# Optimization experiments

Measured on AMD Instinct MI355X. Metric: run time of the kernel, lower is better.

The kernel has to match this reference:

```python
import jax, jax.numpy as jnp
import numpy as np
import math

D = 1024
B, S = 4, 4096


def setup_inputs() -> dict:
    key = jax.random.key(0)
    ks = jax.random.split(key, 8)
    x = jax.random.normal(ks[0], (B, S, D), dtype=jnp.float32)
    W_omega = jax.random.normal(ks[1], (D, D), dtype=jnp.float32) * (1.0 / math.sqrt(D))
    b_omega = jnp.zeros((D,), dtype=jnp.float32)
    log_scale = jnp.full((D,), math.log(0.1), dtype=jnp.float32)
    ln_gamma = jnp.ones((4 * D,), dtype=jnp.float32)
    ln_beta = jnp.zeros((4 * D,), dtype=jnp.float32)
    W1 = jax.random.normal(ks[2], (4 * D, 2 * D), dtype=jnp.float32) * (1.0 / math.sqrt(4 * D))
    b1 = jnp.zeros((2 * D,), dtype=jnp.float32)
    W2 = jax.random.normal(ks[3], (2 * D, D), dtype=jnp.float32) * (1.0 / math.sqrt(2 * D))
    b2 = jnp.zeros((D,), dtype=jnp.float32)
    return {"x": x, "W_omega": W_omega, "b_omega": b_omega, "log_scale": log_scale,
            "ln_gamma": ln_gamma, "ln_beta": ln_beta, "W1": W1, "b1": b1, "W2": W2, "b2": b2}


def _layernorm(x, gamma, beta, eps=1e-5):
    mu = jnp.mean(x, axis=-1, keepdims=True)
    var = jnp.var(x, axis=-1, keepdims=True)
    return (x - mu) * jax.lax.rsqrt(var + eps) * gamma + beta


def reference(x, W_omega, b_omega, log_scale, ln_gamma, ln_beta, W1, b1, W2, b2):
    # x: (B, S, D)
    seq_len = x.shape[1]
    omega = jnp.einsum('bsd,de->bse', x, W_omega) + b_omega
    position = jnp.arange(1, seq_len + 1, dtype=x.dtype)[None, :, None]  # (1,S,1)
    pos_scale = 1.0 / jnp.sqrt(position)
    scale = jnp.exp(log_scale)
    omega_scaled = omega * scale * pos_scale
    phi = jnp.cumsum(omega_scaled, axis=1)
    cos_phi = jnp.cos(phi)
    sin_phi = jnp.sin(phi)
    content_real = x * cos_phi
    content_imag = x * sin_phi
    mem_real = jnp.cumsum(content_real, axis=1) / position
    mem_imag = jnp.cumsum(content_imag, axis=1) / position
    retrieved_real = mem_real * cos_phi + mem_imag * sin_phi
    retrieved_imag = mem_imag * cos_phi - mem_real * sin_phi
    context = jnp.concatenate([content_real, content_imag, retrieved_real, retrieved_imag], axis=-1)
    h = _layernorm(context, ln_gamma, ln_beta)
    h = jnp.einsum('bsf,fg->bsg', h, W1) + b1
    h = jax.nn.gelu(h, approximate=False)  # torch GELU default is exact erf
    # dropout is identity in eval mode
    phase_contribution = jnp.einsum('bsg,gd->bsd', h, W2) + b2
    return x + phase_contribution
```

## Files before the change

kernel.cpp:

```cpp
#include <hip/hip_runtime.h>
#include <hip/hip_bf16.h>
#include <math.h>

typedef __hip_bfloat16 bf16;
typedef __attribute__((ext_vector_type(8))) short bf16x8;
typedef __attribute__((ext_vector_type(4))) float f32x4;

static constexpr int DD = 1024;
static constexpr int BB = 4;
static constexpr int SS = 4096;
static constexpr int FD = 4096;
static constexpr int GDIM = 2048;
static constexpr long SD = (long)SS * DD;
static constexpr long SD4 = 4 * SD;

__device__ __forceinline__ void gl2lds16(const bf16* g, bf16* l) {
    __builtin_amdgcn_global_load_lds(
        (const __attribute__((address_space(1))) void*)g,
        (__attribute__((address_space(3))) void*)l, 16, 0, 0);
}

template <int EPI>
__global__ __launch_bounds__(512, 2) void gemm256(
    const bf16* __restrict__ A, const bf16* __restrict__ BT, void* __restrict__ Cp,
    const float* __restrict__ bias, const float* __restrict__ Xadd,
    int M, int N, int K, long strA, long strBT, long strC)
{
    extern __shared__ bf16 lds[];
    const int tid = threadIdx.x;
    const int l = tid & 63, wv = tid >> 6;
    const int wr = wv >> 2, wc = wv & 3;

    int lin = blockIdx.y * gridDim.x + blockIdx.x;
    {
        const int nwg = gridDim.x * gridDim.y;
        const int qq = nwg >> 3, rr = nwg & 7;
        const int xcd = lin & 7, idx = lin >> 3;
        lin = (xcd < rr ? xcd * (qq + 1) : rr * (qq + 1) + (xcd - rr) * qq) + idx;
    }
    const long m0 = (long)(lin / gridDim.x) * 256;
    const long n0 = (long)(lin % gridDim.x) * 256;

    A += (long)blockIdx.z * strA;
    BT += (long)blockIdx.z * strBT;

    const int schunk = (tid & 3) ^ ((tid >> 3) & 3);
    const bf16* pa = A + (m0 + (tid >> 2)) * (long)K + schunk * 8;
    const bf16* pb = BT + (n0 + (tid >> 2)) * (long)K + schunk * 8;
    const long rowK = 128L * (long)K;
    const int stgOff = wv * 512;

    const int fm = l & 15, q = l >> 4;
    const int lof = fm * 32 + ((q ^ ((fm >> 1) & 3)) * 8);

    f32x4 acc[8][4];
#pragma unroll
    for (int i = 0; i < 8; ++i)
#pragma unroll
        for (int j = 0; j < 4; ++j) acc[i][j] = (f32x4){0.f, 0.f, 0.f, 0.f};

    const int NT = K >> 6;

    {
        bf16* dA0 = lds + stgOff;
        bf16* dA1 = lds + 8192 + stgOff;
        bf16* dB0 = lds + 32768 + stgOff;
        bf16* dB1 = lds + 40960 + stgOff;
        gl2lds16(pa, dA0);       gl2lds16(pa + rowK, dA0 + 4096);
        gl2lds16(pb, dB0);       gl2lds16(pb + rowK, dB0 + 4096);
        gl2lds16(pa + 32, dA1);  gl2lds16(pa + 32 + rowK, dA1 + 4096);
        gl2lds16(pb + 32, dB1);  gl2lds16(pb + 32 + rowK, dB1 + 4096);
        asm volatile("s_waitcnt vmcnt(4)" ::: "memory");
        __builtin_amdgcn_s_barrier();
    }

    for (int t = 0; t < NT; ++t) {
        const int buf = t & 1;
        const bool more = (t + 1) < NT;
        const long ko = (long)(t + 1) * 64;
        const bf16* As0 = lds + buf * 16384;
        const bf16* As1 = As0 + 8192;
        const bf16* Bs0 = lds + 32768 + buf * 16384;
        const bf16* Bs1 = Bs0 + 8192;
        bf16* nA0 = lds + (buf ^ 1) * 16384 + stgOff;
        bf16* nA1 = nA0 + 8192;
        bf16* nB0 = lds + 32768 + (buf ^ 1) * 16384 + stgOff;
        bf16* nB1 = nB0 + 8192;

        {
            const bf16* bb = Bs0 + (wc * 64) * 32 + lof;
            const bf16* ab = As0 + (wr * 128) * 32 + lof;
            bf16x8 bq[4], a0[4], a1[4];
#pragma unroll
            for (int j = 0; j < 4; ++j) bq[j] = *(const bf16x8*)(bb + j * 512);
#pragma unroll
            for (int i = 0; i < 4; ++i) a0[i] = *(const bf16x8*)(ab + i * 512);
#pragma unroll
            for (int i = 0; i < 4; ++i) a1[i] = *(const bf16x8*)(ab + 64 * 32 + i * 512);
            if (more) {
                gl2lds16(pa + ko, nA0); gl2lds16(pa + ko + rowK, nA0 + 4096);
                gl2lds16(pb + ko, nB0); gl2lds16(pb + ko + rowK, nB0 + 4096);
            }
            __builtin_amdgcn_s_setprio(1);
#pragma unroll
            for (int i = 0; i < 4; ++i)
#pragma unroll
                for (int j = 0; j < 4; ++j)
                    acc[i][j] = __builtin_amdgcn_mfma_f32_16x16x32_bf16(a0[i], bq[j], acc[i][j], 0, 0, 0);
            __builtin_amdgcn_s_setprio(0);
            if (more) { gl2lds16(pa + ko + 32, nA1); gl2lds16(pa + ko + 32 + rowK, nA1 + 4096); }
            __builtin_amdgcn_s_setprio(1);
#pragma unroll
            for (int i = 0; i < 4; ++i)
#pragma unroll
                for (int j = 0; j < 4; ++j)
                    acc[4 + i][j] = __builtin_amdgcn_mfma_f32_16x16x32_bf16(a1[i], bq[j], acc[4 + i][j], 0, 0, 0);
            __builtin_amdgcn_s_setprio(0);
        }
        if (more) asm volatile("s_waitcnt vmcnt(6)" ::: "memory");
        else      asm volatile("s_waitcnt vmcnt(0)" ::: "memory");
        __builtin_amdgcn_s_barrier();

        {
            const bf16* bb = Bs1 + (wc * 64) * 32 + lof;
            const bf16* ab = As1 + (wr * 128) * 32 + lof;
            bf16x8 bq[4], a0[4], a1[4];
#pragma unroll
            for (int j = 0; j < 4; ++j) bq[j] = *(const bf16x8*)(bb + j * 512);
#pragma unroll
            for (int i = 0; i < 4; ++i) a0[i] = *(const bf16x8*)(ab + i * 512);
#pragma unroll
            for (int i = 0; i < 4; ++i) a1[i] = *(const bf16x8*)(ab + 64 * 32 + i * 512);
            if (more) { gl2lds16(pb + ko + 32, nB1); gl2lds16(pb + ko + 32 + rowK, nB1 + 4096); }
            __builtin_amdgcn_s_setprio(1);
#pragma unroll
            for (int i = 0; i < 4; ++i)
#pragma unroll
                for (int j = 0; j < 4; ++j)
                    acc[i][j] = __builtin_amdgcn_mfma_f32_16x16x32_bf16(a0[i], bq[j], acc[i][j], 0, 0, 0);
            __builtin_amdgcn_s_setprio(0);
            __builtin_amdgcn_s_setprio(1);
#pragma unroll
            for (int i = 0; i < 4; ++i)
#pragma unroll
                for (int j = 0; j < 4; ++j)
                    acc[4 + i][j] = __builtin_amdgcn_mfma_f32_16x16x32_bf16(a1[i], bq[j], acc[4 + i][j], 0, 0, 0);
            __builtin_amdgcn_s_setprio(0);
        }
        if (more) {
            asm volatile("s_waitcnt vmcnt(4)" ::: "memory");
            __builtin_amdgcn_s_barrier();
        }
    }

    const long cb = (long)blockIdx.z * strC;
#pragma unroll
    for (int i = 0; i < 8; ++i) {
        const long rB = m0 + wr * 128 + i * 16 + q * 4;
#pragma unroll
        for (int j = 0; j < 4; ++j) {
            const long col = n0 + wc * 64 + j * 16 + fm;
#pragma unroll
            for (int r2 = 0; r2 < 4; ++r2) {
                const long row = rB + r2;
                float v = acc[i][j][r2];
                if (EPI == 0) {
                    v += bias[row];
                    ((bf16*)Cp)[cb + row * (long)N + col] = __float2bfloat16(v);
                } else if (EPI == 1) {
                    v += bias[col];
                    v = 0.5f * v * (1.0f + erff(v * 0.70710678118654752f));
                    ((bf16*)Cp)[cb + row * (long)N + col] = __float2bfloat16(v);
                } else {
                    v += bias[col] + Xadd[row * (long)N + col];
                    ((float*)Cp)[cb + row * (long)N + col] = v;
                }
            }
        }
    }
}

__global__ void conv_bf16(const float* __restrict__ in, bf16* __restrict__ out, long n) {
    long i = ((long)blockIdx.x * 256 + threadIdx.x) * 4;
    if (i >= n) return;
    const float4 v = *(const float4*)(in + i);
    bf16 o[4] = {__float2bfloat16(v.x), __float2bfloat16(v.y),
                 __float2bfloat16(v.z), __float2bfloat16(v.w)};
    *(uint2*)(out + i) = *(uint2*)o;
}

__global__ void transpose_f32_bf16(const float* __restrict__ in, bf16* __restrict__ out,
                                   int R, int C, long inStr, long outStr) {
    __shared__ float tl[64][65];
    const float* ip = in + (long)blockIdx.z * inStr;
    bf16* op = out + (long)blockIdx.z * outStr;
    const int r0 = blockIdx.y * 64, c0 = blockIdx.x * 64;
    const int tr = threadIdx.x >> 6, tc = threadIdx.x & 63;
#pragma unroll
    for (int k = 0; k < 16; k++) {
        int r = k * 4 + tr;
        tl[r][tc] = ip[(long)(r0 + r) * C + c0 + tc];
    }
    __syncthreads();
#pragma unroll
    for (int k = 0; k < 16; k++) {
        int r = k * 4 + tr;
        op[(long)(c0 + r) * R + r0 + tc] = __float2bfloat16(tl[tc][r]);
    }
}

__global__ __launch_bounds__(256) void scan_kernel(
    const bf16* __restrict__ omegaT, const bf16* __restrict__ xT,
    const float* __restrict__ log_scale, bf16* __restrict__ ctx,
    long strIn, long strCtx)
{
    const int d = blockIdx.x * 4 + (threadIdx.x >> 6);
    const int lane = threadIdx.x & 63;
    const float sc = expf(log_scale[d]);
    const bf16* po = omegaT + (long)blockIdx.z * strIn + (long)d * SS;
    const bf16* px = xT + (long)blockIdx.z * strIn + (long)d * SS;
    bf16* pc = ctx + (long)blockIdx.z * strCtx + (long)d * SS;

    float phi_c = 0.f, mr_c = 0.f, mi_c = 0.f;
    for (int tchunk = 0; tchunk < SS / 64; tchunk++) {
        const int s = tchunk * 64 + lane;
        const float pos = (float)(s + 1);
        float w = __bfloat162float(po[s]) * sc * rsqrtf(pos);
#pragma unroll
        for (int dlt = 1; dlt < 64; dlt <<= 1) {
            float v = __shfl_up(w, dlt, 64);
            if (lane >= dlt) w += v;
        }
        const float phi = phi_c + w;
        float sph, cph;
        sincosf(phi, &sph, &cph);
        const float xv = __bfloat162float(px[s]);
        const float cr = xv * cph, ci = xv * sph;
        float crs = cr, cis = ci;
#pragma unroll
        for (int dlt = 1; dlt < 64; dlt <<= 1) {
            float v1 = __shfl_up(crs, dlt, 64);
            float v2 = __shfl_up(cis, dlt, 64);
            if (lane >= dlt) { crs += v1; cis += v2; }
        }
        const float invp = 1.0f / pos;
        const float mr = (mr_c + crs) * invp;
        const float mi = (mi_c + cis) * invp;
        const float rr = mr * cph + mi * sph;
        const float ri = mi * cph - mr * sph;
        pc[s] = __float2bfloat16(cr);
        pc[(long)DD * SS + s] = __float2bfloat16(ci);
        pc[2L * DD * SS + s] = __float2bfloat16(rr);
        pc[3L * DD * SS + s] = __float2bfloat16(ri);
        phi_c += __shfl(w, 63, 64);
        mr_c += __shfl(crs, 63, 64);
        mi_c += __shfl(cis, 63, 64);
    }
}

__global__ void zero_f32(float* p, int n) {
    int i = blockIdx.x * 256 + threadIdx.x;
    if (i < n) p[i] = 0.f;
}

__global__ void stats_kernel(const bf16* __restrict__ ctx, float* __restrict__ sums,
                             float* __restrict__ sqs) {
    const int s = blockIdx.x * 256 + threadIdx.x;
    const int f0 = blockIdx.y * 512;
    const int z = blockIdx.z;
    const bf16* p = ctx + (long)z * SD4 + (long)f0 * SS + s;
    float sm = 0.f, sq = 0.f;
    for (int f = 0; f < 512; f++) {
        float v = __bfloat162float(p[(long)f * SS]);
        sm += v;
        sq += v * v;
    }
    atomicAdd(&sums[z * SS + s], sm);
    atomicAdd(&sqs[z * SS + s], sq);
}

__global__ __launch_bounds__(256) void lnt_pair(
    bf16* __restrict__ ctx, const float* __restrict__ sums, const float* __restrict__ sqs,
    const float* __restrict__ gamma, const float* __restrict__ beta)
{
    __shared__ float tA[64][65];
    __shared__ float tB[64][65];
    const int z = blockIdx.z;
    int rem = blockIdx.x, a = 0;
    for (int i = 0; i < 64; i++) {
        int cnt = 64 - i;
        if (rem < cnt) { a = i; break; }
        rem -= cnt;
    }
    const int b = a + rem;
    bf16* base = ctx + (long)z * SD4;
    const int tr = threadIdx.x >> 6, tc = threadIdx.x & 63;
    const float* sums_z = sums + z * SS;
    const float* sqs_z = sqs + z * SS;

#pragma unroll
    for (int k = 0; k < 16; k++) {
        int i = k * 4 + tr;
        tA[i][tc] = __bfloat162float(base[(long)(a * 64 + i) * SS + b * 64 + tc]);
    }
    if (a != b) {
#pragma unroll
        for (int k = 0; k < 16; k++) {
            int i = k * 4 + tr;
            tB[i][tc] = __bfloat162float(base[(long)(b * 64 + i) * SS + a * 64 + tc]);
        }
    }
    __syncthreads();

    {
        const float g = gamma[a * 64 + tc], be = beta[a * 64 + tc];
#pragma unroll
        for (int k = 0; k < 16; k++) {
            const int i = k * 4 + tr;
            const int s = b * 64 + i;
            const float mu = sums_z[s] * (1.0f / FD);
            const float var = sqs_z[s] * (1.0f / FD) - mu * mu;
            const float is = rsqrtf(var + 1e-5f);
            const float v = (tA[tc][i] - mu) * is * g + be;
            base[(long)s * FD + a * 64 + tc] = __float2bfloat16(v);
        }
    }
    if (a != b) {
        const float g = gamma[b * 64 + tc], be = beta[b * 64 + tc];
#pragma unroll
        for (int k = 0; k < 16; k++) {
            const int i = k * 4 + tr;
            const int s = a * 64 + i;
            const float mu = sums_z[s] * (1.0f / FD);
            const float var = sqs_z[s] * (1.0f / FD) - mu * mu;
            const float is = rsqrtf(var + 1e-5f);
            const float v = (tB[tc][i] - mu) * is * g + be;
            base[(long)s * FD + b * 64 + tc] = __float2bfloat16(v);
        }
    }
}

extern "C" void kernel_launch(void* const* d_in, const int* in_sizes, int n_in,
                              void* d_out, int out_size, void* d_ws, size_t ws_size,
                              hipStream_t stream)
{
    const float* x = (const float*)d_in[0];
    const float* Wo = (const float*)d_in[1];
    const float* bo = (const float*)d_in[2];
    const float* lsc = (const float*)d_in[3];
    const float* gam = (const float*)d_in[4];
    const float* bet = (const float*)d_in[5];
    const float* W1 = (const float*)d_in[6];
    const float* b1 = (const float*)d_in[7];
    const float* W2 = (const float*)d_in[8];
    const float* b2 = (const float*)d_in[9];

    static bool attr_done = false;
    if (!attr_done) {
        hipFuncSetAttribute(reinterpret_cast<const void*>(gemm256<0>),
                            hipFuncAttributeMaxDynamicSharedMemorySize, 131072);
        hipFuncSetAttribute(reinterpret_cast<const void*>(gemm256<1>),
                            hipFuncAttributeMaxDynamicSharedMemorySize, 131072);
        hipFuncSetAttribute(reinterpret_cast<const void*>(gemm256<2>),
                            hipFuncAttributeMaxDynamicSharedMemorySize, 131072);
        attr_done = true;
    }

    char* ws = (char*)d_ws;
    const size_t MB = 1024 * 1024;

    bf16* W1T = (bf16*)(ws + 0);
    bf16* W2T = (bf16*)(ws + 16 * MB);
    bf16* WoT = (bf16*)(ws + 20 * MB);
    float* sums = (float*)(ws + 22 * MB);
    float* sqs = sums + 4 * SS;

    transpose_f32_bf16<<<dim3(DD / 64, DD / 64, 1), 256, 0, stream>>>(Wo, WoT, DD, DD, 0, 0);
    transpose_f32_bf16<<<dim3(GDIM / 64, FD / 64, 1), 256, 0, stream>>>(W1, W1T, FD, GDIM, 0, 0);
    transpose_f32_bf16<<<dim3(DD / 64, GDIM / 64, 1), 256, 0, stream>>>(W2, W2T, GDIM, DD, 0, 0);

    const int NPAIR = 64 * 65 / 2;

    if (ws_size >= 220 * MB) {
        bf16* xT  = (bf16*)(ws + 23 * MB);
        bf16* omT = (bf16*)(ws + 55 * MB);
        bf16* ctx = (bf16*)(ws + 87 * MB);
        bf16* xb  = (bf16*)(ws + 87 * MB);
        bf16* h1  = (bf16*)(ws + 23 * MB);

        conv_bf16<<<(int)(BB * SD / 1024), 256, 0, stream>>>(x, xb, BB * SD);
        transpose_f32_bf16<<<dim3(DD / 64, SS / 64, BB), 256, 0, stream>>>(x, xT, SS, DD, SD, SD);

        gemm256<0><<<dim3(SS / 256, DD / 256, BB), 512, 131072, stream>>>(
            WoT, xb, omT, bo, nullptr, DD, SS, DD, 0L, SD, SD);

        scan_kernel<<<dim3(DD / 4, 1, BB), 256, 0, stream>>>(omT, xT, lsc, ctx, SD, SD4);

        zero_f32<<<(8 * SS + 255) / 256, 256, 0, stream>>>(sums, 8 * SS);
        stats_kernel<<<dim3(SS / 256, FD / 512, BB), 256, 0, stream>>>(ctx, sums, sqs);

        lnt_pair<<<dim3(NPAIR, 1, BB), 256, 0, stream>>>(ctx, sums, sqs, gam, bet);

        gemm256<1><<<dim3(GDIM / 256, BB * SS / 256, 1), 512, 131072, stream>>>(
            ctx, W1T, h1, b1, nullptr, BB * SS, GDIM, FD, 0L, 0L, 0L);

        gemm256<2><<<dim3(DD / 256, BB * SS / 256, 1), 512, 131072, stream>>>(
            h1, W2T, d_out, b2, x, BB * SS, DD, GDIM, 0L, 0L, 0L);
    } else {
        bf16* xb  = (bf16*)(ws + 23 * MB);
        bf16* ctx = (bf16*)(ws + 23 * MB);
        bf16* omT = (bf16*)(ws + 55 * MB);
        bf16* xT  = (bf16*)(ws + 63 * MB);
        bf16* h1  = (bf16*)(ws + 55 * MB);

        for (int b = 0; b < BB; b++) {
            const float* xbf = x + (long)b * SD;
            conv_bf16<<<(int)(SD / 1024), 256, 0, stream>>>(xbf, xb, SD);
            transpose_f32_bf16<<<dim3(DD / 64, SS / 64, 1), 256, 0, stream>>>(xbf, xT, SS, DD, 0, 0);
            gemm256<0><<<dim3(SS / 256, DD / 256, 1), 512, 131072, stream>>>(
                WoT, xb, omT, bo, nullptr, DD, SS, DD, 0L, 0L, 0L);
            scan_kernel<<<dim3(DD / 4, 1, 1), 256, 0, stream>>>(omT, xT, lsc, ctx, 0L, 0L);
            zero_f32<<<(2 * SS + 255) / 256, 256, 0, stream>>>(sums, 2 * SS);
            stats_kernel<<<dim3(SS / 256, FD / 512, 1), 256, 0, stream>>>(ctx, sums, sqs);
            lnt_pair<<<dim3(NPAIR, 1, 1), 256, 0, stream>>>(ctx, sums, sqs, gam, bet);
            gemm256<1><<<dim3(GDIM / 256, SS / 256, 1), 512, 131072, stream>>>(
                ctx, W1T, h1, b1, nullptr, SS, GDIM, FD, 0L, 0L, 0L);
            gemm256<2><<<dim3(DD / 256, SS / 256, 1), 512, 131072, stream>>>(
                h1, W2T, (float*)d_out + (long)b * SD, b2, xbf, SS, DD, GDIM, 0L, 0L, 0L);
        }
    }
}
```

Baseline: 756.0 us.

## Shrink GEMM to 256x128 tiles with 4 waves and K-step 32

The 8-wave 256x256 GEMM with 64-wide K steps and split half-tile prefetch is replaced by a 4-wave kernel. It computes 256x128 tiles with 32-wide K steps and a single double-buffered stage, using 48 KB of LDS instead of 128 KB. The aim is to raise occupancy and block count, simplify the pipeline and reduce LDS pressure. In exchange there is less reuse per tile, twice as many K iterations each with a full vmcnt(0) wait and barrier, and more global traffic for the shared operand.

New measurement: 753.8 us. About the same (-0.3%).

```diff
diff --git a/kernel.cpp b/kernel.cpp
--- a/kernel.cpp
+++ b/kernel.cpp
@@ -21,7 +21,7 @@
 }
 
 template <int EPI>
-__global__ __launch_bounds__(512, 2) void gemm256(
+__global__ __launch_bounds__(256, 2) void gemm4w(
     const bf16* __restrict__ A, const bf16* __restrict__ BT, void* __restrict__ Cp,
     const float* __restrict__ bias, const float* __restrict__ Xadd,
     int M, int N, int K, long strA, long strBT, long strC)
@@ -29,7 +29,7 @@
     extern __shared__ bf16 lds[];
     const int tid = threadIdx.x;
     const int l = tid & 63, wv = tid >> 6;
-    const int wr = wv >> 2, wc = wv & 3;
+    const int wr = wv >> 1, wc = wv & 1;
 
     int lin = blockIdx.y * gridDim.x + blockIdx.x;
     {
@@ -39,7 +39,7 @@
         lin = (xcd < rr ? xcd * (qq + 1) : rr * (qq + 1) + (xcd - rr) * qq) + idx;
     }
     const long m0 = (long)(lin / gridDim.x) * 256;
-    const long n0 = (long)(lin % gridDim.x) * 256;
+    const long n0 = (long)(lin % gridDim.x) * 128;
 
     A += (long)blockIdx.z * strA;
     BT += (long)blockIdx.z * strBT;
@@ -47,7 +47,7 @@
     const int schunk = (tid & 3) ^ ((tid >> 3) & 3);
     const bf16* pa = A + (m0 + (tid >> 2)) * (long)K + schunk * 8;
     const bf16* pb = BT + (n0 + (tid >> 2)) * (long)K + schunk * 8;
-    const long rowK = 128L * (long)K;
+    const long row64 = 64L * (long)K;
     const int stgOff = wv * 512;
 
     const int fm = l & 15, q = l >> 4;
@@ -59,96 +59,53 @@
 #pragma unroll
         for (int j = 0; j < 4; ++j) acc[i][j] = (f32x4){0.f, 0.f, 0.f, 0.f};
 
-    const int NT = K >> 6;
+    const int NT = K >> 5;
 
     {
-        bf16* dA0 = lds + stgOff;
-        bf16* dA1 = lds + 8192 + stgOff;
-        bf16* dB0 = lds + 32768 + stgOff;
-        bf16* dB1 = lds + 40960 + stgOff;
-        gl2lds16(pa, dA0);       gl2lds16(pa + rowK, dA0 + 4096);
-        gl2lds16(pb, dB0);       gl2lds16(pb + rowK, dB0 + 4096);
-        gl2lds16(pa + 32, dA1);  gl2lds16(pa + 32 + rowK, dA1 + 4096);
-        gl2lds16(pb + 32, dB1);  gl2lds16(pb + 32 + rowK, dB1 + 4096);
-        asm volatile("s_waitcnt vmcnt(4)" ::: "memory");
+        bf16* dA = lds + stgOff;
+        bf16* dB = lds + 16384 + stgOff;
+        gl2lds16(pa, dA);                gl2lds16(pa + row64, dA + 2048);
+        gl2lds16(pa + 2 * row64, dA + 4096);  gl2lds16(pa + 3 * row64, dA + 6144);
+        gl2lds16(pb, dB);                gl2lds16(pb + row64, dB + 2048);
+        asm volatile("s_waitcnt vmcnt(0)" ::: "memory");
         __builtin_amdgcn_s_barrier();
     }
 
     for (int t = 0; t < NT; ++t) {
         const int buf = t & 1;
         const bool more = (t + 1) < NT;
-        const long ko = (long)(t + 1) * 64;
-        const bf16* As0 = lds + buf * 16384;
-        const bf16* As1 = As0 + 8192;
-        const bf16* Bs0 = lds + 32768 + buf * 16384;
-        const bf16* Bs1 = Bs0 + 8192;
-        bf16* nA0 = lds + (buf ^ 1) * 16384 + stgOff;
-        bf16* nA1 = nA0 + 8192;
-        bf16* nB0 = lds + 32768 + (buf ^ 1) * 16384 + stgOff;
-        bf16* nB1 = nB0 + 8192;
-
+        const long ko = (long)(t + 1) * 32;
+        const bf16* Ab = lds + buf * 8192;
+        const bf16* Bb = lds + 16384 + buf * 4096;
+
+        if (more) {
+            bf16* dA = lds + (buf ^ 1) * 8192 + stgOff;
+            bf16* dB = lds + 16384 + (buf ^ 1) * 4096 + stgOff;
+            gl2lds16(pa + ko, dA);                gl2lds16(pa + ko + row64, dA + 2048);
+            gl2lds16(pa + ko + 2 * row64, dA + 4096);  gl2lds16(pa + ko + 3 * row64, dA + 6144);
+            gl2lds16(pb + ko, dB);                gl2lds16(pb + ko + row64, dB + 2048);
+        }
+
+        bf16x8 bq[4], af[8];
         {
-            const bf16* bb = Bs0 + (wc * 64) * 32 + lof;
-            const bf16* ab = As0 + (wr * 128) * 32 + lof;
-            bf16x8 bq[4], a0[4], a1[4];
+            const bf16* bb = Bb + (wc * 64) * 32 + lof;
+            const bf16* ab = Ab + (wr * 128) * 32 + lof;
 #pragma unroll
             for (int j = 0; j < 4; ++j) bq[j] = *(const bf16x8*)(bb + j * 512);
 #pragma unroll
-            for (int i = 0; i < 4; ++i) a0[i] = *(const bf16x8*)(ab + i * 512);
-#pragma unroll
-            for (int i = 0; i < 4; ++i) a1[i] = *(const bf16x8*)(ab + 64 * 32 + i * 512);
-            if (more) {
-                gl2lds16(pa + ko, nA0); gl2lds16(pa + ko + rowK, nA0 + 4096);
-                gl2lds16(pb + ko, nB0); gl2lds16(pb + ko + rowK, nB0 + 4096);
-            }
-            __builtin_amdgcn_s_setprio(1);
-#pragma unroll
-            for (int i = 0; i < 4; ++i)
-#pragma unroll
-                for (int j = 0; j < 4; ++j)
-                    acc[i][j] = __builtin_amdgcn_mfma_f32_16x16x32_bf16(a0[i], bq[j], acc[i][j], 0, 0, 0);
-            __builtin_amdgcn_s_setprio(0);
-            if (more) { gl2lds16(pa + ko + 32, nA1); gl2lds16(pa + ko + 32 + rowK, nA1 + 4096); }
-            __builtin_amdgcn_s_setprio(1);
-#pragma unroll
-            for (int i = 0; i < 4; ++i)
-#pragma unroll
-                for (int j = 0; j < 4; ++j)
-                    acc[4 + i][j] = __builtin_amdgcn_mfma_f32_16x16x32_bf16(a1[i], bq[j], acc[4 + i][j], 0, 0, 0);
-            __builtin_amdgcn_s_setprio(0);
-        }
-        if (more) asm volatile("s_waitcnt vmcnt(6)" ::: "memory");
-        else      asm volatile("s_waitcnt vmcnt(0)" ::: "memory");
-        __builtin_amdgcn_s_barrier();
-
-        {
-            const bf16* bb = Bs1 + (wc * 64) * 32 + lof;
-            const bf16* ab = As1 + (wr * 128) * 32 + lof;
-            bf16x8 bq[4], a0[4], a1[4];
-#pragma unroll
-            for (int j = 0; j < 4; ++j) bq[j] = *(const bf16x8*)(bb + j * 512);
-#pragma unroll
-            for (int i = 0; i < 4; ++i) a0[i] = *(const bf16x8*)(ab + i * 512);
-#pragma unroll
-            for (int i = 0; i < 4; ++i) a1[i] = *(const bf16x8*)(ab + 64 * 32 + i * 512);
-            if (more) { gl2lds16(pb + ko + 32, nB1); gl2lds16(pb + ko + 32 + rowK, nB1 + 4096); }
-            __builtin_amdgcn_s_setprio(1);
-#pragma unroll
-            for (int i = 0; i < 4; ++i)
-#pragma unroll
-                for (int j = 0; j < 4; ++j)
-                    acc[i][j] = __builtin_amdgcn_mfma_f32_16x16x32_bf16(a0[i], bq[j], acc[i][j], 0, 0, 0);
-            __builtin_amdgcn_s_setprio(0);
-            __builtin_amdgcn_s_setprio(1);
-#pragma unroll
-            for (int i = 0; i < 4; ++i)
-#pragma unroll
-                for (int j = 0; j < 4; ++j)
-                    acc[4 + i][j] = __builtin_amdgcn_mfma_f32_16x16x32_bf16(a1[i], bq[j], acc[4 + i][j], 0, 0, 0);
-            __builtin_amdgcn_s_setprio(0);
-        }
+            for (int i = 0; i < 8; ++i) af[i] = *(const bf16x8*)(ab + i * 512);
+        }
+
+        __builtin_amdgcn_s_setprio(1);
+#pragma unroll
+        for (int i = 0; i < 8; ++i)
+#pragma unroll
+            for (int j = 0; j < 4; ++j)
+                acc[i][j] = __builtin_amdgcn_mfma_f32_16x16x32_bf16(af[i], bq[j], acc[i][j], 0, 0, 0);
+        __builtin_amdgcn_s_setprio(0);
+
         if (more) {
-            asm volatile("s_waitcnt vmcnt(4)" ::: "memory");
+            asm volatile("s_waitcnt vmcnt(0)" ::: "memory");
             __builtin_amdgcn_s_barrier();
         }
     }
@@ -357,12 +314,12 @@
 
     static bool attr_done = false;
     if (!attr_done) {
-        hipFuncSetAttribute(reinterpret_cast<const void*>(gemm256<0>),
-                            hipFuncAttributeMaxDynamicSharedMemorySize, 131072);
-        hipFuncSetAttribute(reinterpret_cast<const void*>(gemm256<1>),
-                            hipFuncAttributeMaxDynamicSharedMemorySize, 131072);
-        hipFuncSetAttribute(reinterpret_cast<const void*>(gemm256<2>),
-                            hipFuncAttributeMaxDynamicSharedMemorySize, 131072);
+        hipFuncSetAttribute(reinterpret_cast<const void*>(gemm4w<0>),
+                            hipFuncAttributeMaxDynamicSharedMemorySize, 49152);
+        hipFuncSetAttribute(reinterpret_cast<const void*>(gemm4w<1>),
+                            hipFuncAttributeMaxDynamicSharedMemorySize, 49152);
+        hipFuncSetAttribute(reinterpret_cast<const void*>(gemm4w<2>),
+                            hipFuncAttributeMaxDynamicSharedMemorySize, 49152);
         attr_done = true;
     }
 
@@ -391,7 +348,7 @@
         conv_bf16<<<(int)(BB * SD / 1024), 256, 0, stream>>>(x, xb, BB * SD);
         transpose_f32_bf16<<<dim3(DD / 64, SS / 64, BB), 256, 0, stream>>>(x, xT, SS, DD, SD, SD);
 
-        gemm256<0><<<dim3(SS / 256, DD / 256, BB), 512, 131072, stream>>>(
+        gemm4w<0><<<dim3(SS / 128, DD / 256, BB), 256, 49152, stream>>>(
             WoT, xb, omT, bo, nullptr, DD, SS, DD, 0L, SD, SD);
 
         scan_kernel<<<dim3(DD / 4, 1, BB), 256, 0, stream>>>(omT, xT, lsc, ctx, SD, SD4);
@@ -401,10 +358,10 @@
 
         lnt_pair<<<dim3(NPAIR, 1, BB), 256, 0, stream>>>(ctx, sums, sqs, gam, bet);
 
-        gemm256<1><<<dim3(GDIM / 256, BB * SS / 256, 1), 512, 131072, stream>>>(
+        gemm4w<1><<<dim3(GDIM / 128, BB * SS / 256, 1), 256, 49152, stream>>>(
             ctx, W1T, h1, b1, nullptr, BB * SS, GDIM, FD, 0L, 0L, 0L);
 
-        gemm256<2><<<dim3(DD / 256, BB * SS / 256, 1), 512, 131072, stream>>>(
+        gemm4w<2><<<dim3(DD / 128, BB * SS / 256, 1), 256, 49152, stream>>>(
             h1, W2T, d_out, b2, x, BB * SS, DD, GDIM, 0L, 0L, 0L);
     } else {
         bf16* xb  = (bf16*)(ws + 23 * MB);
@@ -417,15 +374,15 @@
             const float* xbf = x + (long)b * SD;
             conv_bf16<<<(int)(SD / 1024), 256, 0, stream>>>(xbf, xb, SD);
             transpose_f32_bf16<<<dim3(DD / 64, SS / 64, 1), 256, 0, stream>>>(xbf, xT, SS, DD, 0, 0);
-            gemm256<0><<<dim3(SS / 256, DD / 256, 1), 512, 131072, stream>>>(
+            gemm4w<0><<<dim3(SS / 128, DD / 256, 1), 256, 49152, stream>>>(
                 WoT, xb, omT, bo, nullptr, DD, SS, DD, 0L, 0L, 0L);
             scan_kernel<<<dim3(DD / 4, 1, 1), 256, 0, stream>>>(omT, xT, lsc, ctx, 0L, 0L);
             zero_f32<<<(2 * SS + 255) / 256, 256, 0, stream>>>(sums, 2 * SS);
             stats_kernel<<<dim3(SS / 256, FD / 512, 1), 256, 0, stream>>>(ctx, sums, sqs);
             lnt_pair<<<dim3(NPAIR, 1, 1), 256, 0, stream>>>(ctx, sums, sqs, gam, bet);
-            gemm256<1><<<dim3(GDIM / 256, SS / 256, 1), 512, 131072, stream>>>(
+            gemm4w<1><<<dim3(GDIM / 128, SS / 256, 1), 256, 49152, stream>>>(
                 ctx, W1T, h1, b1, nullptr, SS, GDIM, FD, 0L, 0L, 0L);
-            gemm256<2><<<dim3(DD / 256, SS / 256, 1), 512, 131072, stream>>>(
+            gemm4w<2><<<dim3(DD / 128, SS / 256, 1), 256, 49152, stream>>>(
                 h1, W2T, (float*)d_out + (long)b * SD, b2, xbf, SS, DD, GDIM, 0L, 0L, 0L);
         }
     }
```

## Switch GEMM to 32x32x16 MFMA tiles and use polynomial erf for GELU

Applied to the files above, without the earlier changes.

Replaces the 16x16x32 bf16 MFMA tiling in the shared GEMM kernel with 32x32x16 MFMA instructions. Each wave now holds 4x2 f32x16 accumulators, and the LDS fragment loads and the epilogue indexing are reworked to match, keeping the existing XOR swizzle. The larger MFMA shape does more work per instruction and needs fewer LDS fragment reads per FLOP. The exact erff in the GELU epilogue is replaced by the Abramowitz-Stegun polynomial (max error about 1.5e-7), and the stats reduction loop is unrolled.

Result: slower. 794.6 us (+5.1%).

```diff
diff --git a/kernel.cpp b/kernel.cpp
--- a/kernel.cpp
+++ b/kernel.cpp
@@ -5,6 +5,7 @@
 typedef __hip_bfloat16 bf16;
 typedef __attribute__((ext_vector_type(8))) short bf16x8;
 typedef __attribute__((ext_vector_type(4))) float f32x4;
+typedef __attribute__((ext_vector_type(16))) float f32x16;
 
 static constexpr int DD = 1024;
 static constexpr int BB = 4;
@@ -18,6 +19,16 @@
     __builtin_amdgcn_global_load_lds(
         (const __attribute__((address_space(1))) void*)g,
         (__attribute__((address_space(3))) void*)l, 16, 0, 0);
+}
+
+__device__ __forceinline__ float gelu_exact(float v) {
+    const float ax = fabsf(v) * 0.70710678118654752f;
+    const float t = 1.0f / (1.0f + 0.3275911f * ax);
+    const float poly = t * (0.254829592f + t * (-0.284496736f +
+                       t * (1.421413741f + t * (-1.453152027f + t * 1.061405429f))));
+    const float er = 1.0f - poly * __expf(-ax * ax);
+    const float erfv = v < 0.f ? -er : er;
+    return 0.5f * v * (1.0f + erfv);
 }
 
 template <int EPI>
@@ -50,14 +61,15 @@
     const long rowK = 128L * (long)K;
     const int stgOff = wv * 512;
 
-    const int fm = l & 15, q = l >> 4;
-    const int lof = fm * 32 + ((q ^ ((fm >> 1) & 3)) * 8);
-
-    f32x4 acc[8][4];
-#pragma unroll
-    for (int i = 0; i < 8; ++i)
-#pragma unroll
-        for (int j = 0; j < 4; ++j) acc[i][j] = (f32x4){0.f, 0.f, 0.f, 0.f};
+    const int r31 = l & 31, kh = l >> 5;
+
+    f32x16 acc[4][2];
+#pragma unroll
+    for (int i = 0; i < 4; ++i)
+#pragma unroll
+        for (int j = 0; j < 2; ++j)
+#pragma unroll
+            for (int r = 0; r < 16; ++r) acc[i][j][r] = 0.f;
 
     const int NT = K >> 6;
 
@@ -88,15 +100,23 @@
         bf16* nB1 = nB0 + 8192;
 
         {
-            const bf16* bb = Bs0 + (wc * 64) * 32 + lof;
-            const bf16* ab = As0 + (wr * 128) * 32 + lof;
-            bf16x8 bq[4], a0[4], a1[4];
-#pragma unroll
-            for (int j = 0; j < 4; ++j) bq[j] = *(const bf16x8*)(bb + j * 512);
-#pragma unroll
-            for (int i = 0; i < 4; ++i) a0[i] = *(const bf16x8*)(ab + i * 512);
-#pragma unroll
-            for (int i = 0; i < 4; ++i) a1[i] = *(const bf16x8*)(ab + 64 * 32 + i * 512);
+            bf16x8 bq[2][2], af[4][2];
+#pragma unroll
+            for (int h = 0; h < 2; ++h)
+#pragma unroll
+                for (int j = 0; j < 2; ++j) {
+                    const int br = wc * 64 + j * 32 + r31;
+                    const int ch = (kh + 2 * h) ^ ((br >> 1) & 3);
+                    bq[j][h] = *(const bf16x8*)(Bs0 + br * 32 + ch * 8);
+                }
+#pragma unroll
+            for (int h = 0; h < 2; ++h)
+#pragma unroll
+                for (int i = 0; i < 4; ++i) {
+                    const int ar = wr * 128 + i * 32 + r31;
+                    const int ch = (kh + 2 * h) ^ ((ar >> 1) & 3);
+                    af[i][h] = *(const bf16x8*)(As0 + ar * 32 + ch * 8);
+                }
             if (more) {
                 gl2lds16(pa + ko, nA0); gl2lds16(pa + ko + rowK, nA0 + 4096);
                 gl2lds16(pb + ko, nB0); gl2lds16(pb + ko + rowK, nB0 + 4096);
@@ -105,16 +125,16 @@
 #pragma unroll
             for (int i = 0; i < 4; ++i)
 #pragma unroll
-                for (int j = 0; j < 4; ++j)
-                    acc[i][j] = __builtin_amdgcn_mfma_f32_16x16x32_bf16(a0[i], bq[j], acc[i][j], 0, 0, 0);
+                for (int j = 0; j < 2; ++j)
+                    acc[i][j] = __builtin_amdgcn_mfma_f32_32x32x16_bf16(af[i][0], bq[j][0], acc[i][j], 0, 0, 0);
             __builtin_amdgcn_s_setprio(0);
             if (more) { gl2lds16(pa + ko + 32, nA1); gl2lds16(pa + ko + 32 + rowK, nA1 + 4096); }
             __builtin_amdgcn_s_setprio(1);
 #pragma unroll
             for (int i = 0; i < 4; ++i)
 #pragma unroll
-                for (int j = 0; j < 4; ++j)
-                    acc[4 + i][j] = __builtin_amdgcn_mfma_f32_16x16x32_bf16(a1[i], bq[j], acc[4 + i][j], 0, 0, 0);
+                for (int j = 0; j < 2; ++j)
+                    acc[i][j] = __builtin_amdgcn_mfma_f32_32x32x16_bf16(af[i][1], bq[j][1], acc[i][j], 0, 0, 0);
             __builtin_amdgcn_s_setprio(0);
         }
         if (more) asm volatile("s_waitcnt vmcnt(6)" ::: "memory");
@@ -122,29 +142,37 @@
         __builtin_amdgcn_s_barrier();
 
         {
-            const bf16* bb = Bs1 + (wc * 64) * 32 + lof;
-            const bf16* ab = As1 + (wr * 128) * 32 + lof;
-            bf16x8 bq[4], a0[4], a1[4];
-#pragma unroll
-            for (int j = 0; j < 4; ++j) bq[j] = *(const bf16x8*)(bb + j * 512);
-#pragma unroll
-            for (int i = 0; i < 4; ++i) a0[i] = *(const bf16x8*)(ab + i * 512);
-#pragma unroll
-            for (int i = 0; i < 4; ++i) a1[i] = *(const bf16x8*)(ab + 64 * 32 + i * 512);
+            bf16x8 bq[2][2], af[4][2];
+#pragma unroll
+            for (int h = 0; h < 2; ++h)
+#pragma unroll
+                for (int j = 0; j < 2; ++j) {
+                    const int br = wc * 64 + j * 32 + r31;
+                    const int ch = (kh + 2 * h) ^ ((br >> 1) & 3);
+                    bq[j][h] = *(const bf16x8*)(Bs1 + br * 32 + ch * 8);
+                }
+#pragma unroll
+            for (int h = 0; h < 2; ++h)
+#pragma unroll
+                for (int i = 0; i < 4; ++i) {
+                    const int ar = wr * 128 + i * 32 + r31;
+                    const int ch = (kh + 2 * h) ^ ((ar >> 1) & 3);
+                    af[i][h] = *(const bf16x8*)(As1 + ar * 32 + ch * 8);
+                }
             if (more) { gl2lds16(pb + ko + 32, nB1); gl2lds16(pb + ko + 32 + rowK, nB1 + 4096); }
             __builtin_amdgcn_s_setprio(1);
 #pragma unroll
             for (int i = 0; i < 4; ++i)
 #pragma unroll
-                for (int j = 0; j < 4; ++j)
-                    acc[i][j] = __builtin_amdgcn_mfma_f32_16x16x32_bf16(a0[i], bq[j], acc[i][j], 0, 0, 0);
+                for (int j = 0; j < 2; ++j)
+                    acc[i][j] = __builtin_amdgcn_mfma_f32_32x32x16_bf16(af[i][0], bq[j][0], acc[i][j], 0, 0, 0);
             __builtin_amdgcn_s_setprio(0);
             __builtin_amdgcn_s_setprio(1);
 #pragma unroll
             for (int i = 0; i < 4; ++i)
 #pragma unroll
-                for (int j = 0; j < 4; ++j)
-                    acc[4 + i][j] = __builtin_amdgcn_mfma_f32_16x16x32_bf16(a1[i], bq[j], acc[4 + i][j], 0, 0, 0);
+                for (int j = 0; j < 2; ++j)
+                    acc[i][j] = __builtin_amdgcn_mfma_f32_32x32x16_bf16(af[i][1], bq[j][1], acc[i][j], 0, 0, 0);
             __builtin_amdgcn_s_setprio(0);
         }
         if (more) {
@@ -155,21 +183,21 @@
 
     const long cb = (long)blockIdx.z * strC;
 #pragma unroll
-    for (int i = 0; i < 8; ++i) {
-        const long rB = m0 + wr * 128 + i * 16 + q * 4;
-#pragma unroll
-        for (int j = 0; j < 4; ++j) {
-            const long col = n0 + wc * 64 + j * 16 + fm;
-#pragma unroll
-            for (int r2 = 0; r2 < 4; ++r2) {
-                const long row = rB + r2;
-                float v = acc[i][j][r2];
+    for (int i = 0; i < 4; ++i) {
+        const long rB = m0 + wr * 128 + i * 32 + 4 * kh;
+#pragma unroll
+        for (int j = 0; j < 2; ++j) {
+            const long col = n0 + wc * 64 + j * 32 + r31;
+#pragma unroll
+            for (int r = 0; r < 16; ++r) {
+                const long row = rB + (r & 3) + 8 * (r >> 2);
+                float v = acc[i][j][r];
                 if (EPI == 0) {
                     v += bias[row];
                     ((bf16*)Cp)[cb + row * (long)N + col] = __float2bfloat16(v);
                 } else if (EPI == 1) {
                     v += bias[col];
-                    v = 0.5f * v * (1.0f + erff(v * 0.70710678118654752f));
+                    v = gelu_exact(v);
                     ((bf16*)Cp)[cb + row * (long)N + col] = __float2bfloat16(v);
                 } else {
                     v += bias[col] + Xadd[row * (long)N + col];
@@ -270,6 +298,7 @@
     const int z = blockIdx.z;
     const bf16* p = ctx + (long)z * SD4 + (long)f0 * SS + s;
     float sm = 0.f, sq = 0.f;
+#pragma unroll 8
     for (int f = 0; f < 512; f++) {
         float v = __bfloat162float(p[(long)f * SS]);
         sm += v;
```

## Fold LayerNorm into W1 GEMM epilogue and write scan output row-major

Applied to the files above, without the earlier changes.

LayerNorm is now folded algebraically into the first MLP GEMM. Gamma is pre-multiplied into the transposed W1, the column vectors u = gamma·W1 and t = beta·W1 are precomputed, and the epilogue applies per-row inverse std and mean*inv_std. The scan kernel now stages outputs through LDS and writes context directly in (s, f) layout, so the separate transpose/normalize pass (lnt_pair) and the strided atomic stats kernel go away. Stats are instead computed by a coalesced per-row reduction. GELU uses an Abramowitz-Stegun erf polynomial in place of erff, and the bf16 rounding of un-normalized context changes numerics slightly.

After: 764.2 us. About the same (+1.1%).

```diff
diff --git a/kernel.cpp b/kernel.cpp
--- a/kernel.cpp
+++ b/kernel.cpp
@@ -20,10 +20,26 @@
         (__attribute__((address_space(3))) void*)l, 16, 0, 0);
 }
 
+__device__ __forceinline__ float gelu_exact(float v) {
+    const float ax = fabsf(v) * 0.70710678118654752f;
+    const float t = 1.0f / (1.0f + 0.3275911f * ax);
+    const float poly = t * (0.254829592f + t * (-0.284496736f +
+                       t * (1.421413741f + t * (-1.453152027f + t * 1.061405429f))));
+    const float er = 1.0f - poly * __expf(-ax * ax);
+    const float erfv = v < 0.f ? -er : er;
+    return 0.5f * v * (1.0f + erfv);
+}
+
+__device__ __forceinline__ float bf2f(unsigned short us) {
+    return __uint_as_float(((unsigned)us) << 16);
+}
+
 template <int EPI>
 __global__ __launch_bounds__(512, 2) void gemm256(
     const bf16* __restrict__ A, const bf16* __restrict__ BT, void* __restrict__ Cp,
     const float* __restrict__ bias, const float* __restrict__ Xadd,
+    const float2* __restrict__ is2, const float* __restrict__ uArr,
+    const float* __restrict__ tArr,
     int M, int N, int K, long strA, long strBT, long strC)
 {
     extern __shared__ bf16 lds[];
@@ -154,22 +170,33 @@
     }
 
     const long cb = (long)blockIdx.z * strC;
+    float uu[4], tb[4];
+    if (EPI == 1) {
+#pragma unroll
+        for (int j = 0; j < 4; ++j) {
+            const long col = n0 + wc * 64 + j * 16 + fm;
+            uu[j] = uArr[col];
+            tb[j] = tArr[col] + bias[col];
+        }
+    }
 #pragma unroll
     for (int i = 0; i < 8; ++i) {
         const long rB = m0 + wr * 128 + i * 16 + q * 4;
 #pragma unroll
-        for (int j = 0; j < 4; ++j) {
-            const long col = n0 + wc * 64 + j * 16 + fm;
-#pragma unroll
-            for (int r2 = 0; r2 < 4; ++r2) {
-                const long row = rB + r2;
+        for (int r2 = 0; r2 < 4; ++r2) {
+            const long row = rB + r2;
+            float2 st;
+            if (EPI == 1) st = is2[row];
+#pragma unroll
+            for (int j = 0; j < 4; ++j) {
+                const long col = n0 + wc * 64 + j * 16 + fm;
                 float v = acc[i][j][r2];
                 if (EPI == 0) {
                     v += bias[row];
                     ((bf16*)Cp)[cb + row * (long)N + col] = __float2bfloat16(v);
                 } else if (EPI == 1) {
-                    v += bias[col];
-                    v = 0.5f * v * (1.0f + erff(v * 0.70710678118654752f));
+                    v = st.x * v - st.y * uu[j] + tb[j];
+                    v = gelu_exact(v);
                     ((bf16*)Cp)[cb + row * (long)N + col] = __float2bfloat16(v);
                 } else {
                     v += bias[col] + Xadd[row * (long)N + col];
@@ -190,7 +217,8 @@
 }
 
 __global__ void transpose_f32_bf16(const float* __restrict__ in, bf16* __restrict__ out,
-                                   int R, int C, long inStr, long outStr) {
+                                   int R, int C, long inStr, long outStr,
+                                   const float* __restrict__ rscale) {
     __shared__ float tl[64][65];
     const float* ip = in + (long)blockIdx.z * inStr;
     bf16* op = out + (long)blockIdx.z * outStr;
@@ -199,7 +227,9 @@
 #pragma unroll
     for (int k = 0; k < 16; k++) {
         int r = k * 4 + tr;
-        tl[r][tc] = ip[(long)(r0 + r) * C + c0 + tc];
+        float v = ip[(long)(r0 + r) * C + c0 + tc];
+        if (rscale) v *= rscale[r0 + r];
+        tl[r][tc] = v;
     }
     __syncthreads();
 #pragma unroll
@@ -209,17 +239,43 @@
     }
 }
 
-__global__ __launch_bounds__(256) void scan_kernel(
+__global__ void zero_f32(float* p, int n) {
+    int i = blockIdx.x * 256 + threadIdx.x;
+    if (i < n) p[i] = 0.f;
+}
+
+__global__ void ut_kernel(const float* __restrict__ W1, const float* __restrict__ gamma,
+                          const float* __restrict__ beta, float* __restrict__ uArr,
+                          float* __restrict__ tArr) {
+    const int g = blockIdx.x * 256 + threadIdx.x;
+    const int f0 = blockIdx.y * 512;
+    float su = 0.f, st = 0.f;
+    for (int f = 0; f < 512; ++f) {
+        const float w = W1[(long)(f0 + f) * GDIM + g];
+        su += gamma[f0 + f] * w;
+        st += beta[f0 + f] * w;
+    }
+    atomicAdd(&uArr[g], su);
+    atomicAdd(&tArr[g], st);
+}
+
+__global__ __launch_bounds__(1024) void scan16(
     const bf16* __restrict__ omegaT, const bf16* __restrict__ xT,
     const float* __restrict__ log_scale, bf16* __restrict__ ctx,
     long strIn, long strCtx)
 {
-    const int d = blockIdx.x * 4 + (threadIdx.x >> 6);
-    const int lane = threadIdx.x & 63;
+    __shared__ bf16 stg[64 * 70];
+    const int tid = threadIdx.x;
+    const int wv = tid >> 6, lane = tid & 63;
+    const int d0 = blockIdx.x * 16;
+    const int d = d0 + wv;
+    const int z = blockIdx.z;
     const float sc = expf(log_scale[d]);
-    const bf16* po = omegaT + (long)blockIdx.z * strIn + (long)d * SS;
-    const bf16* px = xT + (long)blockIdx.z * strIn + (long)d * SS;
-    bf16* pc = ctx + (long)blockIdx.z * strCtx + (long)d * SS;
+    const bf16* po = omegaT + (long)z * strIn + (long)d * SS;
+    const bf16* px = xT + (long)z * strIn + (long)d * SS;
+    bf16* pc = ctx + (long)z * strCtx;
+    const int so_i = tid >> 4;
+    const int so_d = tid & 15;
 
     float phi_c = 0.f, mr_c = 0.f, mi_c = 0.f;
     for (int tchunk = 0; tchunk < SS / 64; tchunk++) {
@@ -248,95 +304,51 @@
         const float mi = (mi_c + cis) * invp;
         const float rr = mr * cph + mi * sph;
         const float ri = mi * cph - mr * sph;
-        pc[s] = __float2bfloat16(cr);
-        pc[(long)DD * SS + s] = __float2bfloat16(ci);
-        pc[2L * DD * SS + s] = __float2bfloat16(rr);
-        pc[3L * DD * SS + s] = __float2bfloat16(ri);
+        stg[lane * 70 +      wv] = __float2bfloat16(cr);
+        stg[lane * 70 + 17 + wv] = __float2bfloat16(ci);
+        stg[lane * 70 + 34 + wv] = __float2bfloat16(rr);
+        stg[lane * 70 + 51 + wv] = __float2bfloat16(ri);
         phi_c += __shfl(w, 63, 64);
         mr_c += __shfl(crs, 63, 64);
         mi_c += __shfl(cis, 63, 64);
-    }
-}
-
-__global__ void zero_f32(float* p, int n) {
-    int i = blockIdx.x * 256 + threadIdx.x;
-    if (i < n) p[i] = 0.f;
-}
-
-__global__ void stats_kernel(const bf16* __restrict__ ctx, float* __restrict__ sums,
-                             float* __restrict__ sqs) {
-    const int s = blockIdx.x * 256 + threadIdx.x;
-    const int f0 = blockIdx.y * 512;
+        __syncthreads();
+        bf16* row = pc + (long)(tchunk * 64 + so_i) * FD + d0 + so_d;
+        row[0]          = stg[so_i * 70 +      so_d];
+        row[DD]         = stg[so_i * 70 + 17 + so_d];
+        row[2 * DD]     = stg[so_i * 70 + 34 + so_d];
+        row[3 * DD]     = stg[so_i * 70 + 51 + so_d];
+        __syncthreads();
+    }
+}
+
+__global__ __launch_bounds__(256) void stats2(
+    const bf16* __restrict__ ctx, float2* __restrict__ is2, long strCtx)
+{
+    const int s = blockIdx.x * 4 + (threadIdx.x >> 6);
+    const int lane = threadIdx.x & 63;
     const int z = blockIdx.z;
-    const bf16* p = ctx + (long)z * SD4 + (long)f0 * SS + s;
+    const bf16* p = ctx + (long)z * strCtx + (long)s * FD;
     float sm = 0.f, sq = 0.f;
-    for (int f = 0; f < 512; f++) {
-        float v = __bfloat162float(p[(long)f * SS]);
-        sm += v;
-        sq += v * v;
-    }
-    atomicAdd(&sums[z * SS + s], sm);
-    atomicAdd(&sqs[z * SS + s], sq);
-}
-
-__global__ __launch_bounds__(256) void lnt_pair(
-    bf16* __restrict__ ctx, const float* __restrict__ sums, const float* __restrict__ sqs,
-    const float* __restrict__ gamma, const float* __restrict__ beta)
-{
-    __shared__ float tA[64][65];
-    __shared__ float tB[64][65];
-    const int z = blockIdx.z;
-    int rem = blockIdx.x, a = 0;
-    for (int i = 0; i < 64; i++) {
-        int cnt = 64 - i;
-        if (rem < cnt) { a = i; break; }
-        rem -= cnt;
-    }
-    const int b = a + rem;
-    bf16* base = ctx + (long)z * SD4;
-    const int tr = threadIdx.x >> 6, tc = threadIdx.x & 63;
-    const float* sums_z = sums + z * SS;
-    const float* sqs_z = sqs + z * SS;
-
-#pragma unroll
-    for (int k = 0; k < 16; k++) {
-        int i = k * 4 + tr;
-        tA[i][tc] = __bfloat162float(base[(long)(a * 64 + i) * SS + b * 64 + tc]);
-    }
-    if (a != b) {
-#pragma unroll
-        for (int k = 0; k < 16; k++) {
-            int i = k * 4 + tr;
-            tB[i][tc] = __bfloat162float(base[(long)(b * 64 + i) * SS + a * 64 + tc]);
-        }
-    }
-    __syncthreads();
-
-    {
-        const float g = gamma[a * 64 + tc], be = beta[a * 64 + tc];
-#pragma unroll
-        for (int k = 0; k < 16; k++) {
-            const int i = k * 4 + tr;
-            const int s = b * 64 + i;
-            const float mu = sums_z[s] * (1.0f / FD);
-            const float var = sqs_z[s] * (1.0f / FD) - mu * mu;
-            const float is = rsqrtf(var + 1e-5f);
-            const float v = (tA[tc][i] - mu) * is * g + be;
-            base[(long)s * FD + a * 64 + tc] = __float2bfloat16(v);
-        }
-    }
-    if (a != b) {
-        const float g = gamma[b * 64 + tc], be = beta[b * 64 + tc];
-#pragma unroll
-        for (int k = 0; k < 16; k++) {
-            const int i = k * 4 + tr;
-            const int s = a * 64 + i;
-            const float mu = sums_z[s] * (1.0f / FD);
-            const float var = sqs_z[s] * (1.0f / FD) - mu * mu;
-            const float is = rsqrtf(var + 1e-5f);
-            const float v = (tB[tc][i] - mu) * is * g + be;
-            base[(long)s * FD + b * 64 + tc] = __float2bfloat16(v);
-        }
+#pragma unroll
+    for (int i = 0; i < 8; ++i) {
+        bf16x8 v8 = *(const bf16x8*)(p + lane * 8 + i * 512);
+#pragma unroll
+        for (int j = 0; j < 8; ++j) {
+            const float v = bf2f((unsigned short)v8[j]);
+            sm += v;
+            sq += v * v;
+        }
+    }
+#pragma unroll
+    for (int o = 1; o < 64; o <<= 1) {
+        sm += __shfl_xor(sm, o, 64);
+        sq += __shfl_xor(sq, o, 64);
+    }
+    if (lane == 0) {
+        const float mu = sm * (1.0f / FD);
+        const float var = sq * (1.0f / FD) - mu * mu;
+        const float is = rsqrtf(var + 1e-5f);
+        is2[z * SS + s] = make_float2(is, is * mu);
     }
 }
 
@@ -369,17 +381,18 @@
     char* ws = (char*)d_ws;
     const size_t MB = 1024 * 1024;
 
-    bf16* W1T = (bf16*)(ws + 0);
+    bf16* W1gT = (bf16*)(ws + 0);
     bf16* W2T = (bf16*)(ws + 16 * MB);
     bf16* WoT = (bf16*)(ws + 20 * MB);
-    float* sums = (float*)(ws + 22 * MB);
-    float* sqs = sums + 4 * SS;
-
-    transpose_f32_bf16<<<dim3(DD / 64, DD / 64, 1), 256, 0, stream>>>(Wo, WoT, DD, DD, 0, 0);
-    transpose_f32_bf16<<<dim3(GDIM / 64, FD / 64, 1), 256, 0, stream>>>(W1, W1T, FD, GDIM, 0, 0);
-    transpose_f32_bf16<<<dim3(DD / 64, GDIM / 64, 1), 256, 0, stream>>>(W2, W2T, GDIM, DD, 0, 0);
-
-    const int NPAIR = 64 * 65 / 2;
+    float2* is2 = (float2*)(ws + 22 * MB);
+    float* uArr = (float*)(ws + 22 * MB + 128 * 1024);
+    float* tArr = (float*)(ws + 22 * MB + 136 * 1024);
+
+    transpose_f32_bf16<<<dim3(DD / 64, DD / 64, 1), 256, 0, stream>>>(Wo, WoT, DD, DD, 0, 0, nullptr);
+    transpose_f32_bf16<<<dim3(GDIM / 64, FD / 64, 1), 256, 0, stream>>>(W1, W1gT, FD, GDIM, 0, 0, gam);
+    transpose_f32_bf16<<<dim3(DD / 64, GDIM / 64, 1), 256, 0, stream>>>(W2, W2T, GDIM, DD, 0, 0, nullptr);
+    zero_f32<<<(2 * GDIM + 255) / 256, 256, 0, stream>>>(uArr, 2 * GDIM);
+    ut_kernel<<<dim3(GDIM / 256, FD / 512, 1), 256, 0, stream>>>(W1, gam, bet, uArr, tArr);
 
     if (ws_size >= 220 * MB) {
         bf16* xT  = (bf16*)(ws + 23 * MB);
@@ -389,23 +402,20 @@
         bf16* h1  = (bf16*)(ws + 23 * MB);
 
         conv_bf16<<<(int)(BB * SD / 1024), 256, 0, stream>>>(x, xb, BB * SD);
-        transpose_f32_bf16<<<dim3(DD / 64, SS / 64, BB), 256, 0, stream>>>(x, xT, SS, DD, SD, SD);
+        transpose_f32_bf16<<<dim3(DD / 64, SS / 64, BB), 256, 0, stream>>>(x, xT, SS, DD, SD, SD, nullptr);
 
         gemm256<0><<<dim3(SS / 256, DD / 256, BB), 512, 131072, stream>>>(
-            WoT, xb, omT, bo, nullptr, DD, SS, DD, 0L, SD, SD);
-
-        scan_kernel<<<dim3(DD / 4, 1, BB), 256, 0, stream>>>(omT, xT, lsc, ctx, SD, SD4);
-
-        zero_f32<<<(8 * SS + 255) / 256, 256, 0, stream>>>(sums, 8 * SS);
-        stats_kernel<<<dim3(SS / 256, FD / 512, BB), 256, 0, stream>>>(ctx, sums, sqs);
-
-        lnt_pair<<<dim3(NPAIR, 1, BB), 256, 0, stream>>>(ctx, sums, sqs, gam, bet);
+            WoT, xb, omT, bo, nullptr, nullptr, nullptr, nullptr, DD, SS, DD, 0L, SD, SD);
+
+        scan16<<<dim3(DD / 16, 1, BB), 1024, 0, stream>>>(omT, xT, lsc, ctx, SD, SD4);
+
+        stats2<<<dim3(SS / 4, 1, BB), 256, 0, stream>>>(ctx, is2, SD4);
 
         gemm256<1><<<dim3(GDIM / 256, BB * SS / 256, 1), 512, 131072, stream>>>(
-            ctx, W1T, h1, b1, nullptr, BB * SS, GDIM, FD, 0L, 0L, 0L);
+            ctx, W1gT, h1, b1, nullptr, is2, uArr, tArr, BB * SS, GDIM, FD, 0L, 0L, 0L);
 
         gemm256<2><<<dim3(DD / 256, BB * SS / 256, 1), 512, 131072, stream>>>(
-            h1, W2T, d_out, b2, x, BB * SS, DD, GDIM, 0L, 0L, 0L);
+            h1, W2T, d_out, b2, x, nullptr, nullptr, nullptr, BB * SS, DD, GDIM, 0L, 0L, 0L);
     } else {
         bf16* xb  = (bf16*)(ws + 23 * MB);
         bf16* ctx = (bf16*)(ws + 23 * MB);
@@ -416,17 +426,16 @@
         for (int b = 0; b < BB; b++) {
             const float* xbf = x + (long)b * SD;
             conv_bf16<<<(int)(SD / 1024), 256, 0, stream>>>(xbf, xb, SD);
-            transpose_f32_bf16<<<dim3(DD / 64, SS / 64, 1), 256, 0, stream>>>(xbf, xT, SS, DD, 0, 0);
+            transpose_f32_bf16<<<dim3(DD / 64, SS / 64, 1), 256, 0, stream>>>(xbf, xT, SS, DD, 0, 0, nullptr);
             gemm256<0><<<dim3(SS / 256, DD / 256, 1), 512, 131072, stream>>>(
-                WoT, xb, omT, bo, nullptr, DD, SS, DD, 0L, 0L, 0L);
-            scan_kernel<<<dim3(DD / 4, 1, 1), 256, 0, stream>>>(omT, xT, lsc, ctx, 0L, 0L);
-            zero_f32<<<(2 * SS + 255) / 256, 256, 0, stream>>>(sums, 2 * SS);
-            stats_kernel<<<dim3(SS / 256, FD / 512, 1), 256, 0, stream>>>(ctx, sums, sqs);
-            lnt_pair<<<dim3(NPAIR, 1, 1), 256, 0, stream>>>(ctx, sums, sqs, gam, bet);
+                WoT, xb, omT, bo, nullptr, nullptr, nullptr, nullptr, DD, SS, DD, 0L, 0L, 0L);
+            scan16<<<dim3(DD / 16, 1, 1), 1024, 0, stream>>>(omT, xT, lsc, ctx, 0L, 0L);
+            stats2<<<dim3(SS / 4, 1, 1), 256, 0, stream>>>(ctx, is2, 0L);
             gemm256<1><<<dim3(GDIM / 256, SS / 256, 1), 512, 131072, stream>>>(
-                ctx, W1T, h1, b1, nullptr, SS, GDIM, FD, 0L, 0L, 0L);
+                ctx, W1gT, h1, b1, nullptr, is2, uArr, tArr, SS, GDIM, FD, 0L, 0L, 0L);
             gemm256<2><<<dim3(DD / 256, SS / 256, 1), 512, 131072, stream>>>(
-                h1, W2T, (float*)d_out + (long)b * SD, b2, xbf, SS, DD, GDIM, 0L, 0L, 0L);
-        }
-    }
-}
+                h1, W2T, (float*)d_out + (long)b * SD, b2, xbf, nullptr, nullptr, nullptr,
+                SS, DD, GDIM, 0L, 0L, 0L);
+        }
+    }
+}
```
